# Performance work log

Measured on AMD Instinct MI355X. Metric: run time of the kernel, lower is better.

## Reference

```python
import jax, jax.numpy as jnp
import numpy as np

E = 800_000      # number of edges
D = 256          # d_model_edge
N = 50_000       # number of atoms/nodes


def setup_inputs() -> dict:
    key = jax.random.key(0)
    k1, k2, k3, k4, k5 = jax.random.split(key, 5)
    forces = jax.random.normal(k1, (E, D), dtype=jnp.float32)
    V_st = jax.random.normal(k2, (E, 3), dtype=jnp.float32)
    # MLP([D, D, 1]): Linear(D,D) + act + Linear(D,1). Scaled init for stability.
    W1 = jax.random.normal(k3, (D, D), dtype=jnp.float32) * (1.0 / np.sqrt(D))
    b1 = jnp.zeros((D,), dtype=jnp.float32)
    W2 = jax.random.normal(k4, (D, 1), dtype=jnp.float32) * (1.0 / np.sqrt(D))
    b2 = jnp.zeros((1,), dtype=jnp.float32)
    idx_t = jax.random.randint(k5, (E,), 0, N, dtype=jnp.int64 if jax.config.jax_enable_x64 else jnp.int32)
    return {
        "forces": forces,
        "V_st": V_st,
        "W1": W1,
        "b1": b1,
        "W2": W2,
        "b2": b2,
        "idx_t": idx_t,
        "n_atoms": N,
    }


def reference(forces, V_st, W1, b1, W2, b2, idx_t, n_atoms):
    # out_mlp: Linear(D,D) -> SiLU -> Linear(D,1)
    h = jax.nn.silu(forces @ W1 + b1)          # [E, D]
    s = h @ W2 + b2                            # [E, 1] per-edge scalar
    ev = s * V_st                              # [E, 3] scaled direction vectors
    # scatter-sum over target node indices (reduction='sum')
    out = jax.ops.segment_sum(ev, idx_t, num_segments=n_atoms)  # [N, 3]
    return out
```

## Files before the change

### kernel.cpp

```cpp
#include <hip/hip_runtime.h>
#include <hip/hip_bf16.h>

typedef __attribute__((ext_vector_type(8))) short short8;
typedef __attribute__((ext_vector_type(4))) float floatx4;
typedef unsigned short u16;

#define D 256
#define BM 128
#define NT 512
#define NBLK 256

__device__ __forceinline__ short f2bf(float f) {
    return __builtin_bit_cast(short, __float2bfloat16(f));
}

__global__ void prep_kernel(const float* __restrict__ W1, u16* __restrict__ W1F,
                            float* __restrict__ out, int outn) {
    const int b = blockIdx.x;
    if (b < D) {
        const int k = b, n = threadIdx.x;
        const int k0t = k >> 5, g = (k >> 3) & 3, j = k & 7;
        const int nt = n >> 4, l15 = n & 15;
        W1F[(long)((((k0t << 4) + nt) << 6) + (g << 4) + l15) * 8 + j] = (u16)f2bf(W1[k * D + n]);
    } else {
        int i = (b - D) * 256 + threadIdx.x;
        const int stride = (gridDim.x - D) * 256;
        for (; i < outn; i += stride) out[i] = 0.f;
    }
}

#define GLOAD_LDS(g, l) __builtin_amdgcn_global_load_lds( \
    (const __attribute__((address_space(1))) unsigned int*)(g), \
    (__attribute__((address_space(3))) unsigned int*)(l), 16, 0, 0)

struct R8 { floatx4 f0, f1; };

__launch_bounds__(NT, 2)
__global__ void head_kernel(const float* __restrict__ forces,
                            const float* __restrict__ V_st,
                            const u16*   __restrict__ W1F,
                            const float* __restrict__ b1,
                            const float* __restrict__ W2,
                            const float* __restrict__ b2,
                            const int*   __restrict__ idx_t,
                            float* __restrict__ out,
                            int E) {
    __shared__ u16 Blds[128 * 512];
    __shared__ u16 Abuf[2][8 * 512];
    __shared__ float s_red[4][BM];

    const int tid  = threadIdx.x;
    const int lane = tid & 63;
    const int w    = tid >> 6;
    const int wm   = w >> 2;
    const int wn   = w & 3;
    const int l15  = lane & 15;
    const int g    = lane >> 4;
    const int ntiles = E / BM;

#pragma unroll
    for (int j = 0; j < 16; ++j) {
        int frag = w * 16 + j;
        GLOAD_LDS(W1F + frag * 512 + lane * 8, &Blds[frag * 512]);
    }

    float b1v[4], w2v[4];
#pragma unroll
    for (int nc = 0; nc < 4; ++nc) {
        int n = wn * 64 + nc * 16 + l15;
        b1v[nc] = b1[n];
        w2v[nc] = W2[n];
    }
    const float b2v = b2[0];

    const int arow = tid >> 2;
    const int agg  = tid & 3;
    const int aoff = (arow >> 4) * 512 + (((agg << 4) | (arow & 15)) * 8);

    auto ISSUE = [&](int cs) -> R8 {
        long t = (long)blockIdx.x + (long)(cs >> 3) * NBLK;
        if (t >= (long)ntiles) t = 0;
        const float* src = forces + (t * BM + arow) * (long)D + (cs & 7) * 32 + agg * 8;
        R8 r;
        r.f0 = *(const floatx4*)src;
        r.f1 = *(const floatx4*)(src + 4);
        return r;
    };
    auto CVTW = [&](int buf, const R8& r) {
        short8 a;
#pragma unroll
        for (int j = 0; j < 4; ++j) { a[j] = f2bf(r.f0[j]); a[4 + j] = f2bf(r.f1[j]); }
        *(short8*)&Abuf[buf][aoff] = a;
    };

    floatx4 acc[4][4];
#pragma unroll
    for (int mr = 0; mr < 4; ++mr)
#pragma unroll
        for (int nc = 0; nc < 4; ++nc)
            acc[mr][nc] = (floatx4){0.f, 0.f, 0.f, 0.f};

    auto COMPUTE = [&](int buf, int k0t) {
        short8 bf[4], af[4];
#pragma unroll
        for (int nc = 0; nc < 4; ++nc)
            bf[nc] = *(const short8*)&Blds[(k0t * 16 + wn * 4 + nc) * 512 + lane * 8];
#pragma unroll
        for (int mr = 0; mr < 4; ++mr)
            af[mr] = *(const short8*)&Abuf[buf][(wm * 4 + mr) * 512 + lane * 8];
#pragma unroll
        for (int mr = 0; mr < 4; ++mr)
#pragma unroll
            for (int nc = 0; nc < 4; ++nc)
                acc[mr][nc] = __builtin_amdgcn_mfma_f32_16x16x32_bf16(
                    af[mr], bf[nc], acc[mr][nc], 0, 0, 0);
    };

    R8 Ra = ISSUE(0);
    R8 Rb = ISSUE(1);
    CVTW(0, Ra);
    __syncthreads();

    int cs = 0;
    for (long t = blockIdx.x; t < (long)ntiles; t += NBLK) {
        float vx = 0.f, vy = 0.f, vz = 0.f;
        int node = -1;
        if (tid < BM) {
            long e = t * BM + tid;
            vx = V_st[e * 3 + 0]; vy = V_st[e * 3 + 1]; vz = V_st[e * 3 + 2];
            node = idx_t[e];
        }

        Ra = ISSUE(cs + 2); COMPUTE(0, 0); CVTW(1, Rb); __syncthreads();
        Rb = ISSUE(cs + 3); COMPUTE(1, 1); CVTW(0, Ra); __syncthreads();
        Ra = ISSUE(cs + 4); COMPUTE(0, 2); CVTW(1, Rb); __syncthreads();
        Rb = ISSUE(cs + 5); COMPUTE(1, 3); CVTW(0, Ra); __syncthreads();
        Ra = ISSUE(cs + 6); COMPUTE(0, 4); CVTW(1, Rb); __syncthreads();
        Rb = ISSUE(cs + 7); COMPUTE(1, 5); CVTW(0, Ra); __syncthreads();
        Ra = ISSUE(cs + 8); COMPUTE(0, 6); CVTW(1, Rb); __syncthreads();
        Rb = ISSUE(cs + 9); COMPUTE(1, 7); CVTW(0, Ra); __syncthreads();
        cs += 8;

        float part[4][4];
#pragma unroll
        for (int mr = 0; mr < 4; ++mr)
#pragma unroll
            for (int r = 0; r < 4; ++r) {
                float sv = 0.f;
#pragma unroll
                for (int nc = 0; nc < 4; ++nc) {
                    float z = acc[mr][nc][r] + b1v[nc];
                    float h = z / (1.f + __expf(-z));
                    sv += h * w2v[nc];
                }
                part[mr][r] = sv;
            }
#pragma unroll
        for (int mr = 0; mr < 4; ++mr)
#pragma unroll
            for (int nc = 0; nc < 4; ++nc)
                acc[mr][nc] = (floatx4){0.f, 0.f, 0.f, 0.f};

#pragma unroll
        for (int off = 1; off < 16; off <<= 1)
#pragma unroll
            for (int mr = 0; mr < 4; ++mr)
#pragma unroll
                for (int r = 0; r < 4; ++r)
                    part[mr][r] += __shfl_xor(part[mr][r], off, 16);

        if (l15 == 0) {
#pragma unroll
            for (int mr = 0; mr < 4; ++mr)
#pragma unroll
                for (int r = 0; r < 4; ++r)
                    s_red[wn][wm * 64 + mr * 16 + g * 4 + r] = part[mr][r];
        }
        __syncthreads();

        if (node >= 0) {
            float sv = s_red[0][tid] + s_red[1][tid] + s_red[2][tid] + s_red[3][tid] + b2v;
            atomicAdd(&out[(long)node * 3 + 0], sv * vx);
            atomicAdd(&out[(long)node * 3 + 1], sv * vy);
            atomicAdd(&out[(long)node * 3 + 2], sv * vz);
        }
    }
}

extern "C" void kernel_launch(void* const* d_in, const int* in_sizes, int n_in,
                              void* d_out, int out_size, void* d_ws, size_t ws_size,
                              hipStream_t stream) {
    const float* forces = (const float*)d_in[0];
    const float* V_st   = (const float*)d_in[1];
    const float* W1     = (const float*)d_in[2];
    const float* b1     = (const float*)d_in[3];
    const float* W2     = (const float*)d_in[4];
    const float* b2     = (const float*)d_in[5];
    const int*   idx    = (const int*)d_in[6];
    const int E = in_sizes[6];

    u16* W1F = (u16*)d_ws;

    prep_kernel<<<D + 128, 256, 0, stream>>>(W1, W1F, (float*)d_out, out_size);
    head_kernel<<<NBLK, NT, 0, stream>>>(forces, V_st, W1F, b1, W2, b2, idx,
                                         (float*)d_out, E);
}
```

Measured before the change: 329.9 us.

## Replace persistent double-buffered kernel with one-tile-per-block, B fragments read from global

Drops the persistent 256-block kernel that staged all of W1 in LDS and double-buffered A chunks. Each block now handles one 64-row tile with 256 threads: it loads the whole A tile to registers, converts it to bf16 into LDS, and reads W1 fragments straight from global/L2 for the MFMA. LDS use per block falls sharply, which allows many more resident blocks and lets the hardware hide memory latency without a software pipeline. The cost is repeated W1 reads from L2 by every block, the loss of load/compute overlap inside a block, and many more block launches.

Result: faster. 282.1 us (-14.5%).

```diff
diff --git a/kernel.cpp b/kernel.cpp
--- a/kernel.cpp
+++ b/kernel.cpp
@@ -6,9 +6,8 @@
 typedef unsigned short u16;
 
 #define D 256
-#define BM 128
-#define NT 512
-#define NBLK 256
+#define BM 64
+#define NT 256
 
 __device__ __forceinline__ short f2bf(float f) {
     return __builtin_bit_cast(short, __float2bfloat16(f));
@@ -29,13 +28,9 @@
     }
 }
 
-#define GLOAD_LDS(g, l) __builtin_amdgcn_global_load_lds( \
-    (const __attribute__((address_space(1))) unsigned int*)(g), \
-    (__attribute__((address_space(3))) unsigned int*)(l), 16, 0, 0)
-
 struct R8 { floatx4 f0, f1; };
 
-__launch_bounds__(NT, 2)
+__launch_bounds__(NT, 4)
 __global__ void head_kernel(const float* __restrict__ forces,
                             const float* __restrict__ V_st,
                             const u16*   __restrict__ W1F,
@@ -45,145 +40,121 @@
                             const int*   __restrict__ idx_t,
                             float* __restrict__ out,
                             int E) {
-    __shared__ u16 Blds[128 * 512];
-    __shared__ u16 Abuf[2][8 * 512];
-    __shared__ float s_red[4][BM];
+    __shared__ u16 Albs[32 * 512];
+    __shared__ float s_red[2][BM];
 
     const int tid  = threadIdx.x;
     const int lane = tid & 63;
     const int w    = tid >> 6;
-    const int wm   = w >> 2;
-    const int wn   = w & 3;
+    const int wm   = w >> 1;
+    const int wn   = w & 1;
     const int l15  = lane & 15;
     const int g    = lane >> 4;
-    const int ntiles = E / BM;
+
+    const long t = blockIdx.x;
+    const long row0 = t * BM;
+
+    float vx = 0.f, vy = 0.f, vz = 0.f;
+    int node = -1;
+    if (tid < BM) {
+        long e = row0 + tid;
+        if (e < E) {
+            vx = V_st[e * 3 + 0]; vy = V_st[e * 3 + 1]; vz = V_st[e * 3 + 2];
+            node = idx_t[e];
+        }
+    }
+
+    const int arow = tid >> 2;
+    const int agg  = tid & 3;
+    long grow = row0 + arow;
+    if (grow > (long)E - 1) grow = (long)E - 1;
+    const float* abase = forces + grow * D + agg * 8;
+
+    R8 r[8];
+#pragma unroll
+    for (int k0t = 0; k0t < 8; ++k0t) {
+        r[k0t].f0 = *(const floatx4*)(abase + k0t * 32);
+        r[k0t].f1 = *(const floatx4*)(abase + k0t * 32 + 4);
+    }
+    const int aslot = ((agg << 4) | (arow & 15)) * 8;
+    const int art   = arow >> 4;
+#pragma unroll
+    for (int k0t = 0; k0t < 8; ++k0t) {
+        short8 a;
+#pragma unroll
+        for (int j = 0; j < 4; ++j) { a[j] = f2bf(r[k0t].f0[j]); a[4 + j] = f2bf(r[k0t].f1[j]); }
+        *(short8*)&Albs[(k0t * 4 + art) * 512 + aslot] = a;
+    }
+    __syncthreads();
+
+    floatx4 acc[2][8];
+#pragma unroll
+    for (int mr = 0; mr < 2; ++mr)
+#pragma unroll
+        for (int nc = 0; nc < 8; ++nc)
+            acc[mr][nc] = (floatx4){0.f, 0.f, 0.f, 0.f};
 
 #pragma unroll
-    for (int j = 0; j < 16; ++j) {
-        int frag = w * 16 + j;
-        GLOAD_LDS(W1F + frag * 512 + lane * 8, &Blds[frag * 512]);
+    for (int k0t = 0; k0t < 8; ++k0t) {
+        short8 bf[8], af[2];
+#pragma unroll
+        for (int nc = 0; nc < 8; ++nc)
+            bf[nc] = *(const short8*)(W1F + (long)((k0t * 16 + wn * 8 + nc) * 64 + lane) * 8);
+#pragma unroll
+        for (int mr = 0; mr < 2; ++mr)
+            af[mr] = *(const short8*)&Albs[(k0t * 4 + wm * 2 + mr) * 512 + lane * 8];
+#pragma unroll
+        for (int mr = 0; mr < 2; ++mr)
+#pragma unroll
+            for (int nc = 0; nc < 8; ++nc)
+                acc[mr][nc] = __builtin_amdgcn_mfma_f32_16x16x32_bf16(
+                    af[mr], bf[nc], acc[mr][nc], 0, 0, 0);
     }
 
-    float b1v[4], w2v[4];
+    float b1v[8], w2v[8];
 #pragma unroll
-    for (int nc = 0; nc < 4; ++nc) {
-        int n = wn * 64 + nc * 16 + l15;
+    for (int nc = 0; nc < 8; ++nc) {
+        int n = wn * 128 + nc * 16 + l15;
         b1v[nc] = b1[n];
         w2v[nc] = W2[n];
     }
-    const float b2v = b2[0];
+    float part[2][4];
+#pragma unroll
+    for (int mr = 0; mr < 2; ++mr)
+#pragma unroll
+        for (int rr = 0; rr < 4; ++rr) {
+            float sv = 0.f;
+#pragma unroll
+            for (int nc = 0; nc < 8; ++nc) {
+                float z = acc[mr][nc][rr] + b1v[nc];
+                float h = z / (1.f + __expf(-z));
+                sv += h * w2v[nc];
+            }
+            part[mr][rr] = sv;
+        }
 
-    const int arow = tid >> 2;
-    const int agg  = tid & 3;
-    const int aoff = (arow >> 4) * 512 + (((agg << 4) | (arow & 15)) * 8);
+#pragma unroll
+    for (int off = 1; off < 16; off <<= 1)
+#pragma unroll
+        for (int mr = 0; mr < 2; ++mr)
+#pragma unroll
+            for (int rr = 0; rr < 4; ++rr)
+                part[mr][rr] += __shfl_xor(part[mr][rr], off, 16);
 
-    auto ISSUE = [&](int cs) -> R8 {
-        long t = (long)blockIdx.x + (long)(cs >> 3) * NBLK;
-        if (t >= (long)ntiles) t = 0;
-        const float* src = forces + (t * BM + arow) * (long)D + (cs & 7) * 32 + agg * 8;
-        R8 r;
-        r.f0 = *(const floatx4*)src;
-        r.f1 = *(const floatx4*)(src + 4);
-        return r;
-    };
-    auto CVTW = [&](int buf, const R8& r) {
-        short8 a;
+    if (l15 == 0) {
 #pragma unroll
-        for (int j = 0; j < 4; ++j) { a[j] = f2bf(r.f0[j]); a[4 + j] = f2bf(r.f1[j]); }
-        *(short8*)&Abuf[buf][aoff] = a;
-    };
-
-    floatx4 acc[4][4];
+        for (int mr = 0; mr < 2; ++mr)
 #pragma unroll
-    for (int mr = 0; mr < 4; ++mr)
-#pragma unroll
-        for (int nc = 0; nc < 4; ++nc)
-            acc[mr][nc] = (floatx4){0.f, 0.f, 0.f, 0.f};
-
-    auto COMPUTE = [&](int buf, int k0t) {
-        short8 bf[4], af[4];
-#pragma unroll
-        for (int nc = 0; nc < 4; ++nc)
-            bf[nc] = *(const short8*)&Blds[(k0t * 16 + wn * 4 + nc) * 512 + lane * 8];
-#pragma unroll
-        for (int mr = 0; mr < 4; ++mr)
-            af[mr] = *(const short8*)&Abuf[buf][(wm * 4 + mr) * 512 + lane * 8];
-#pragma unroll
-        for (int mr = 0; mr < 4; ++mr)
-#pragma unroll
-            for (int nc = 0; nc < 4; ++nc)
-                acc[mr][nc] = __builtin_amdgcn_mfma_f32_16x16x32_bf16(
-                    af[mr], bf[nc], acc[mr][nc], 0, 0, 0);
-    };
-
-    R8 Ra = ISSUE(0);
-    R8 Rb = ISSUE(1);
-    CVTW(0, Ra);
+            for (int rr = 0; rr < 4; ++rr)
+                s_red[wn][wm * 32 + mr * 16 + g * 4 + rr] = part[mr][rr];
+    }
     __syncthreads();
 
-    int cs = 0;
-    for (long t = blockIdx.x; t < (long)ntiles; t += NBLK) {
-        float vx = 0.f, vy = 0.f, vz = 0.f;
-        int node = -1;
-        if (tid < BM) {
-            long e = t * BM + tid;
-            vx = V_st[e * 3 + 0]; vy = V_st[e * 3 + 1]; vz = V_st[e * 3 + 2];
-            node = idx_t[e];
-        }
-
-        Ra = ISSUE(cs + 2); COMPUTE(0, 0); CVTW(1, Rb); __syncthreads();
-        Rb = ISSUE(cs + 3); COMPUTE(1, 1); CVTW(0, Ra); __syncthreads();
-        Ra = ISSUE(cs + 4); COMPUTE(0, 2); CVTW(1, Rb); __syncthreads();
-        Rb = ISSUE(cs + 5); COMPUTE(1, 3); CVTW(0, Ra); __syncthreads();
-        Ra = ISSUE(cs + 6); COMPUTE(0, 4); CVTW(1, Rb); __syncthreads();
-        Rb = ISSUE(cs + 7); COMPUTE(1, 5); CVTW(0, Ra); __syncthreads();
-        Ra = ISSUE(cs + 8); COMPUTE(0, 6); CVTW(1, Rb); __syncthreads();
-        Rb = ISSUE(cs + 9); COMPUTE(1, 7); CVTW(0, Ra); __syncthreads();
-        cs += 8;
-
-        float part[4][4];
-#pragma unroll
-        for (int mr = 0; mr < 4; ++mr)
-#pragma unroll
-            for (int r = 0; r < 4; ++r) {
-                float sv = 0.f;
-#pragma unroll
-                for (int nc = 0; nc < 4; ++nc) {
-                    float z = acc[mr][nc][r] + b1v[nc];
-                    float h = z / (1.f + __expf(-z));
-                    sv += h * w2v[nc];
-                }
-                part[mr][r] = sv;
-            }
-#pragma unroll
-        for (int mr = 0; mr < 4; ++mr)
-#pragma unroll
-            for (int nc = 0; nc < 4; ++nc)
-                acc[mr][nc] = (floatx4){0.f, 0.f, 0.f, 0.f};
-
-#pragma unroll
-        for (int off = 1; off < 16; off <<= 1)
-#pragma unroll
-            for (int mr = 0; mr < 4; ++mr)
-#pragma unroll
-                for (int r = 0; r < 4; ++r)
-                    part[mr][r] += __shfl_xor(part[mr][r], off, 16);
-
-        if (l15 == 0) {
-#pragma unroll
-            for (int mr = 0; mr < 4; ++mr)
-#pragma unroll
-                for (int r = 0; r < 4; ++r)
-                    s_red[wn][wm * 64 + mr * 16 + g * 4 + r] = part[mr][r];
-        }
-        __syncthreads();
-
-        if (node >= 0) {
-            float sv = s_red[0][tid] + s_red[1][tid] + s_red[2][tid] + s_red[3][tid] + b2v;
-            atomicAdd(&out[(long)node * 3 + 0], sv * vx);
-            atomicAdd(&out[(long)node * 3 + 1], sv * vy);
-            atomicAdd(&out[(long)node * 3 + 2], sv * vz);
-        }
+    if (node >= 0) {
+        float sv = s_red[0][tid] + s_red[1][tid] + b2[0];
+        atomicAdd(&out[(long)node * 3 + 0], sv * vx);
+        atomicAdd(&out[(long)node * 3 + 1], sv * vy);
+        atomicAdd(&out[(long)node * 3 + 2], sv * vz);
     }
 }
 
@@ -202,6 +173,7 @@
     u16* W1F = (u16*)d_ws;
 
     prep_kernel<<<D + 128, 256, 0, stream>>>(W1, W1F, (float*)d_out, out_size);
-    head_kernel<<<NBLK, NT, 0, stream>>>(forces, V_st, W1F, b1, W2, b2, idx,
+    const int grid = (E + BM - 1) / BM;
+    head_kernel<<<grid, NT, 0, stream>>>(forces, V_st, W1F, b1, W2, b2, idx,
                                          (float*)d_out, E);
 }
```
